# Kernel tuning notes

Hardware: AMD Instinct MI355X
Metric: run time of the kernel (lower is better)

## Reference

```python
import jax, jax.numpy as jnp
import numpy as np
from jax import lax

IMG_SIZE = 640
STRIDES = (8, 16, 32)
NA = 3          # anchors per level
NC = 80         # classes
CONF_THRESH = 0.001
NMS_THRESH = 0.6
ANCHORS = np.array([[10,13],[16,30],[33,23],[30,61],[62,45],[59,119],[116,90],[156,198],[373,326]], np.float32).reshape(3, 3, 2)

def _make_grids():
    gs, st, aw = [], [], []
    for i, s in enumerate(STRIDES):
        hs = ws = IMG_SIZE // s
        gy, gx = np.meshgrid(np.arange(hs), np.arange(ws), indexing='ij')
        gxy = np.stack([gx, gy], -1).astype(np.float32).reshape(1, hs*ws, 1, 2)
        gs.append(gxy)
        st.append(np.full((1, hs*ws, NA, 2), s, np.float32))
        aw.append(np.tile(ANCHORS[i][None], (hs*ws, 1, 1)))
    return (np.concatenate(gs, 1), np.concatenate(st, 1), np.concatenate(aw, 0)[None])

GRID_CELL, STRIDE_T, ANCH_WH = _make_grids()  # [1,HW,1,2], [1,HW,3,2], [1,HW,3,2]

def _nms_classaware(boxes, score, valid):
    # Greedy NMS, class-aware via coordinate offset already applied to boxes.
    # Faithful to the numpy baseline: w,h = max(1e-28, .), areas without +1.
    x1, y1, x2, y2 = boxes[:, 0], boxes[:, 1], boxes[:, 2], boxes[:, 3]
    areas = (x2 - x1) * (y2 - y1)
    order = jnp.argsort(-score)
    N = boxes.shape[0]
    def body(i, state):
        supp, keep = state
        idx = order[i]
        active = jnp.logical_and(jnp.logical_not(supp[idx]), valid[idx])
        keep = keep.at[idx].set(active)
        xx1 = jnp.maximum(x1[idx], x1)
        yy1 = jnp.maximum(y1[idx], y1)
        xx2 = jnp.minimum(x2[idx], x2)
        yy2 = jnp.minimum(y2[idx], y2)
        w = jnp.maximum(1e-28, xx2 - xx1)
        h = jnp.maximum(1e-28, yy2 - yy1)
        inter = w * h
        iou = inter / (areas[idx] + areas - inter)
        newsupp = jnp.logical_and(iou > NMS_THRESH, active)
        newsupp = newsupp.at[idx].set(False)
        return jnp.logical_or(supp, newsupp), keep
    supp0 = jnp.zeros((N,), bool)
    keep0 = jnp.zeros((N,), bool)
    _, keep = lax.fori_loop(0, N, body, (supp0, keep0))
    return keep

def _decode_and_nms(pred_s, pred_m, pred_l):
    objs, clss, regs = [], [], []
    for pred in (pred_s, pred_m, pred_l):
        B, C, H, W = pred.shape
        p = pred.transpose(0, 2, 3, 1).reshape(B, H*W, C)
        objs.append(p[..., :NA].reshape(B, H*W*NA, 1))
        clss.append(p[..., NA:NA*(1+NC)].reshape(B, H*W*NA, NC))
        regs.append(p[..., NA*(1+NC):].reshape(B, H*W, NA, 4))
    obj_pred = jnp.concatenate(objs, axis=1)   # [B, N, 1]
    cls_pred = jnp.concatenate(clss, axis=1)   # [B, N, NC]
    reg_pred = jnp.concatenate(regs, axis=1)   # [B, HW, 3, 4]
    grid = jnp.asarray(GRID_CELL)
    stride = jnp.asarray(STRIDE_T)
    anch = jnp.asarray(ANCH_WH)
    B = reg_pred.shape[0]
    c_xy = (jax.nn.sigmoid(reg_pred[..., :2]) + grid) * stride
    b_wh = jnp.exp(reg_pred[..., 2:]) * anch
    xywh = jnp.concatenate([c_xy, b_wh], -1).reshape(B, -1, 4)
    x1y1 = xywh[..., :2] - xywh[..., 2:] / 2
    x2y2 = xywh[..., :2] + xywh[..., 2:] / 2
    boxes = jnp.clip(jnp.concatenate([x1y1, x2y2], -1) / IMG_SIZE, 0.0, 1.0)[0]  # [N,4]
    obj_s = jax.nn.sigmoid(obj_pred)[0]                     # [N,1]
    scores_all = jax.nn.softmax(cls_pred[0], axis=1) * obj_s  # [N,NC]
    cls_ind = jnp.argmax(scores_all, axis=1)                # [N]
    score = jnp.max(scores_all, axis=1)                     # [N]
    valid = score >= CONF_THRESH
    # class-aware NMS: offset normalized boxes by 2*class so classes never overlap
    boxes_off = boxes + cls_ind[:, None].astype(boxes.dtype) * 2.0
    keep = _nms_classaware(lax.stop_gradient(boxes_off), lax.stop_gradient(score), valid)
    out = jnp.concatenate([
        boxes,                                    # 4 cols
        score[:, None],                           # 1 col
        cls_ind[:, None].astype(boxes.dtype),     # 1 col (non-diff)
        keep[:, None].astype(boxes.dtype),        # 1 col (non-diff)
    ], axis=1)                                    # [N, 7]
    return out

def setup_inputs() -> dict:
    key = jax.random.key(0)
    k1, k2, k3 = jax.random.split(key, 3)
    return {
        'pred_s': jax.random.normal(k1, (1, 255, 80, 80), jnp.float32),
        'pred_m': jax.random.normal(k2, (1, 255, 40, 40), jnp.float32),
        'pred_l': jax.random.normal(k3, (1, 255, 20, 20), jnp.float32),
    }

def reference(pred_s, pred_m, pred_l):
    return _decode_and_nms(pred_s, pred_m, pred_l)
```

## Files before the change

kernel.cpp:

```cpp
#include <hip/hip_runtime.h>
#include <cstdint>

#define NPRED 25200
#define NPOS  8400
#define NCLS  80
#define CAP   512
#define CSTRIDE 16
#define MW    8
#define NCHUNK 132

__device__ __forceinline__ float sigmoidf_(float x) { return 1.0f / (1.0f + expf(-x)); }

__global__ __launch_bounds__(64) void decode_kernel(
    const float* __restrict__ ps, const float* __restrict__ pm, const float* __restrict__ pl,
    float* __restrict__ out, int* __restrict__ counts,
    float4* __restrict__ g_boxin, uint64_t* __restrict__ g_key)
{
    int chunk = blockIdx.x;
    int a     = blockIdx.y;
    int t     = threadIdx.x;

    const float* p; int HW, W, base, si; float stride; int w0;
    if (chunk < 100)      { p = ps; HW = 6400; W = 80; stride = 8.f;  base = 0;    si = 0; w0 = chunk * 64; }
    else if (chunk < 125) { p = pm; HW = 1600; W = 40; stride = 16.f; base = 6400; si = 1; w0 = (chunk - 100) * 64; }
    else                  { p = pl; HW = 400;  W = 20; stride = 32.f; base = 8000; si = 2; w0 = (chunk - 125) * 64; }

    int local = w0 + t;
    bool valid = local < HW;
    int lclamp = valid ? local : (HW - 1);

    __shared__ float lds[NCLS * 64];

    const float* cbase = p + (size_t)(3 + a * NCLS) * HW;
    int lane_c = t >> 4;
    int j      = (t & 15) << 2;
    int off    = w0 + j; if (off > HW - 4) off = HW - 4;

    float4 vreg[20];
#pragma unroll
    for (int r0 = 0; r0 < 20; r0++)
        vreg[r0] = *(const float4*)(cbase + (size_t)(r0 * 4 + lane_c) * HW + off);
    float objl = p[(size_t)a * HW + lclamp];
    const float* rb = p + (size_t)(3 + 3 * NCLS + a * 4) * HW + lclamp;
    float tx = rb[0], ty = rb[(size_t)HW], tw = rb[(size_t)2 * HW], th = rb[(size_t)3 * HW];
#pragma unroll
    for (int r0 = 0; r0 < 20; r0++)
        *(float4*)&lds[(r0 * 4 + lane_c) * 64 + j] = vreg[r0];
    __syncthreads();

    float m = -INFINITY;
#pragma unroll 16
    for (int c = 0; c < NCLS; c++) m = fmaxf(m, lds[c * 64 + t]);
    float s = 0.f;
#pragma unroll 16
    for (int c = 0; c < NCLS; c++) {
        float e = expf(lds[c * 64 + t] - m);
        lds[c * 64 + t] = e;
        s += e;
    }
    float obj = sigmoidf_(objl);
    float best = -1.f; int bi = 0;
#pragma unroll 16
    for (int c = 0; c < NCLS; c++) {
        float sc = lds[c * 64 + t] / s * obj;
        if (sc > best) { best = sc; bi = c; }
    }

    if (!valid) return;

    const float AW[9] = {10.f,16.f,33.f, 30.f,62.f,59.f, 116.f,156.f,373.f};
    const float AH[9] = {13.f,30.f,23.f, 61.f,45.f,119.f, 90.f,198.f,326.f};
    float aw = AW[si*3 + a], ah = AH[si*3 + a];

    int y = local / W;
    int x = local - y * W;
    float cx = (sigmoidf_(tx) + (float)x) * stride;
    float cy = (sigmoidf_(ty) + (float)y) * stride;
    float bw = expf(tw) * aw;
    float bh = expf(th) * ah;
    float x1 = fminf(fmaxf((cx - bw / 2.f) / 640.f, 0.f), 1.f);
    float y1 = fminf(fmaxf((cy - bh / 2.f) / 640.f, 0.f), 1.f);
    float x2 = fminf(fmaxf((cx + bw / 2.f) / 640.f, 0.f), 1.f);
    float y2 = fminf(fmaxf((cy + bh / 2.f) / 640.f, 0.f), 1.f);

    int g = (base + local) * 3 + a;
    float clsf = (float)bi;
    float* o = out + (size_t)g * 7;
    o[0] = x1; o[1] = y1; o[2] = x2; o[3] = y2;
    o[4] = best; o[5] = clsf; o[6] = 0.f;

    if (best >= 0.001f) {
        int slot = atomicAdd(&counts[bi * CSTRIDE], 1);
        if (slot < CAP) {
            float off2 = clsf * 2.0f;
            g_boxin[bi * CAP + slot] = make_float4(x1 + off2, y1 + off2,
                                                   x2 + off2, y2 + off2);
            unsigned u = __float_as_uint(best);
            u = (u & 0x80000000u) ? ~u : (u | 0x80000000u);
            g_key[bi * CAP + slot] = ((uint64_t)(~u) << 15) | (uint64_t)g;
        }
    }
}

__global__ __launch_bounds__(1024) void nms_fused_kernel(
    const int* __restrict__ counts, const uint64_t* __restrict__ g_key,
    const float4* __restrict__ g_boxin, float* __restrict__ out)
{
    int c = blockIdx.x;
    int n = counts[c * CSTRIDE]; if (n > CAP) n = CAP;
    if (n == 0) return;
    int tid = threadIdx.x;
    int nw = (n + 63) >> 6;

    __shared__ uint64_t key_s[CAP];
    __shared__ float4   boxu_s[CAP];
    __shared__ float4   sbox_s[CAP + 64];
    __shared__ int      sg_s[CAP];
    __shared__ uint64_t mask_s[MW * CAP];

    for (int i = tid; i < n; i += 1024) {
        key_s[i]  = g_key[c * CAP + i];
        boxu_s[i] = g_boxin[c * CAP + i];
    }
    for (int i = n + tid; i < n + 64; i += 1024)
        sbox_s[i] = make_float4(3e30f, 3e30f, 3e30f, 3e30f);
    __syncthreads();

    for (int i0 = 0; i0 < n; i0 += 256) {
        int item = i0 + (tid >> 2);
        int sub  = tid & 3;
        bool act = item < n;
        int r = 0;
        uint64_t k = 0;
        if (act) {
            k = key_s[item];
            int nq = (n + 3) >> 2;
            int lo = sub * nq; if (lo > n) lo = n;
            int hi = lo + nq;  if (hi > n) hi = n;
            int jj = lo;
            for (; jj + 8 <= hi; jj += 8) {
                int t0 = key_s[jj]   < k, t1 = key_s[jj+1] < k;
                int t2 = key_s[jj+2] < k, t3 = key_s[jj+3] < k;
                int t4 = key_s[jj+4] < k, t5 = key_s[jj+5] < k;
                int t6 = key_s[jj+6] < k, t7 = key_s[jj+7] < k;
                r += t0 + t1 + t2 + t3 + t4 + t5 + t6 + t7;
            }
            for (; jj < hi; jj++) r += (key_s[jj] < k);
        }
        r += __shfl_xor(r, 1);
        r += __shfl_xor(r, 2);
        if (act && sub == 0) {
            sbox_s[r] = boxu_s[item];
            sg_s[r]   = (int)(k & 0x7FFF);
        }
    }
    __syncthreads();

    {
        int wid   = tid >> 6;
        int lane2 = tid & 63;
        int T = nw * (nw + 1) / 2;
        for (int t = wid; t < T; t += 16) {
            int w = 0, acc = 0;
            while (t >= acc + w + 1) { acc += w + 1; w++; }
            int ib = t - acc;
            int i  = (ib << 6) + lane2;
            float4 b4 = sbox_s[i];
            float Ai = (b4.z - b4.x) * (b4.w - b4.y);
            int j0 = w << 6;
            uint64_t bits = 0;
#pragma unroll 8
            for (int jq = 0; jq < 64; jq++) {
                float4 bj = sbox_s[j0 + jq];
                float xx1 = fmaxf(b4.x, bj.x);
                float yy1 = fmaxf(b4.y, bj.y);
                float xx2 = fminf(b4.z, bj.z);
                float yy2 = fminf(b4.w, bj.w);
                float ww = fmaxf(1e-28f, xx2 - xx1);
                float hh = fmaxf(1e-28f, yy2 - yy1);
                float inter = ww * hh;
                float Aj = (bj.z - bj.x) * (bj.w - bj.y);
                float iou = inter / ((Ai + Aj) - inter);
                if ((j0 + jq) > i && iou > 0.6f) bits |= 1ull << jq;
            }
            if (i < n) mask_s[w * CAP + i] = bits;
        }
    }
    __syncthreads();

    if (tid >= 64) return;
    int lane = tid;
    uint64_t removed = 0;
    for (int w = 0; w < nw; w++) {
        uint64_t rw = __shfl(removed, w);
        int row = (w << 6) + lane;
        uint64_t diag = (row < n) ? mask_s[w * CAP + row] : 0ull;
        int rem = n - (w << 6);
        uint64_t valid = (rem >= 64) ? ~0ull : ((1ull << rem) - 1ull);
        uint64_t nulls = __ballot(diag == 0ull);
        uint64_t cand = ~rw & valid;
        uint64_t kw = 0;
        uint64_t it = cand & ~nulls;
        while (it) {
            int b = __ffsll((unsigned long long)it) - 1;
            kw |= 1ull << b;
            uint64_t db = __shfl(diag, b);
            it &= ~db; cand &= ~db;
            it &= ~(1ull << b);
        }
        kw |= cand & nulls;

        int g  = lane >> 3;
        int wp = lane & 7;
        uint64_t acc = 0;
        if (wp >= w && wp < nw) {
            uint64_t mybits = kw & (0xFFull << (g * 8));
            while (mybits) {
                int b = __ffsll((unsigned long long)mybits) - 1;
                mybits &= mybits - 1;
                acc |= mask_s[wp * CAP + ((w << 6) + b)];
            }
        }
        acc |= __shfl_xor(acc, 8);
        acc |= __shfl_xor(acc, 16);
        acc |= __shfl_xor(acc, 32);
        if (lane < MW) removed |= acc;

        if (row < n && ((kw >> lane) & 1))
            out[(size_t)sg_s[row] * 7 + 6] = 1.0f;
    }
}

extern "C" void kernel_launch(void* const* d_in, const int* in_sizes, int n_in,
                              void* d_out, int out_size, void* d_ws, size_t ws_size,
                              hipStream_t stream) {
    const float* ps = (const float*)d_in[0];
    const float* pm = (const float*)d_in[1];
    const float* pl = (const float*)d_in[2];
    float* out = (float*)d_out;

    char* ws = (char*)d_ws;
    int*      counts  = (int*)ws;
    float4*   g_boxin = (float4*)(ws + 8192);
    uint64_t* g_key   = (uint64_t*)(ws + 663552);

    hipMemsetAsync(counts, 0, 8192, stream);
    decode_kernel<<<dim3(NCHUNK, 3), 64, 0, stream>>>(ps, pm, pl, out, counts, g_boxin, g_key);
    nms_fused_kernel<<<NCLS, 1024, 0, stream>>>(counts, g_key, g_boxin, out);
}
```

Baseline: 111.9 us.

## Replace global atomic class bucketing with per-class scan in NMS kernel

Decode now writes every prediction's key, with the class packed into the high bits, plus its box into dense arrays indexed by prediction id. This removes the global atomic counters and the memset launch. Each NMS block then scans all 25200 keys, compacts its own class into shared memory with an LDS atomic, and gathers boxes by index. The trade is one fewer launch and no global atomic contention, at the cost of every block reading the full key array (about 200KB per block, 80 blocks).

```diff
diff --git a/kernel.cpp b/kernel.cpp
--- a/kernel.cpp
+++ b/kernel.cpp
@@ -5,7 +5,6 @@
 #define NPOS  8400
 #define NCLS  80
 #define CAP   512
-#define CSTRIDE 16
 #define MW    8
 #define NCHUNK 132
 
@@ -13,7 +12,7 @@
 
 __global__ __launch_bounds__(64) void decode_kernel(
     const float* __restrict__ ps, const float* __restrict__ pm, const float* __restrict__ pl,
-    float* __restrict__ out, int* __restrict__ counts,
+    float* __restrict__ out,
     float4* __restrict__ g_boxin, uint64_t* __restrict__ g_key)
 {
     int chunk = blockIdx.x;
@@ -90,38 +89,47 @@
     o[4] = best; o[5] = clsf; o[6] = 0.f;
 
     if (best >= 0.001f) {
-        int slot = atomicAdd(&counts[bi * CSTRIDE], 1);
-        if (slot < CAP) {
-            float off2 = clsf * 2.0f;
-            g_boxin[bi * CAP + slot] = make_float4(x1 + off2, y1 + off2,
-                                                   x2 + off2, y2 + off2);
-            unsigned u = __float_as_uint(best);
-            u = (u & 0x80000000u) ? ~u : (u | 0x80000000u);
-            g_key[bi * CAP + slot] = ((uint64_t)(~u) << 15) | (uint64_t)g;
-        }
+        float off2 = clsf * 2.0f;
+        g_boxin[g] = make_float4(x1 + off2, y1 + off2, x2 + off2, y2 + off2);
+        unsigned u = __float_as_uint(best);
+        u = (u & 0x80000000u) ? ~u : (u | 0x80000000u);
+        g_key[g] = ((uint64_t)bi << 47) | ((uint64_t)(~u) << 15) | (uint64_t)g;
+    } else {
+        g_key[g] = (uint64_t)127 << 47;
     }
 }
 
 __global__ __launch_bounds__(1024) void nms_fused_kernel(
-    const int* __restrict__ counts, const uint64_t* __restrict__ g_key,
-    const float4* __restrict__ g_boxin, float* __restrict__ out)
+    const uint64_t* __restrict__ g_key, const float4* __restrict__ g_boxin,
+    float* __restrict__ out)
 {
     int c = blockIdx.x;
-    int n = counts[c * CSTRIDE]; if (n > CAP) n = CAP;
-    if (n == 0) return;
     int tid = threadIdx.x;
-    int nw = (n + 63) >> 6;
 
     __shared__ uint64_t key_s[CAP];
     __shared__ float4   boxu_s[CAP];
     __shared__ float4   sbox_s[CAP + 64];
     __shared__ int      sg_s[CAP];
     __shared__ uint64_t mask_s[MW * CAP];
-
-    for (int i = tid; i < n; i += 1024) {
-        key_s[i]  = g_key[c * CAP + i];
-        boxu_s[i] = g_boxin[c * CAP + i];
-    }
+    __shared__ int      ln_s;
+
+    if (tid == 0) ln_s = 0;
+    __syncthreads();
+
+    for (int idx = tid; idx < NPRED; idx += 1024) {
+        uint64_t k = g_key[idx];
+        if ((int)(k >> 47) == c) {
+            int slot = atomicAdd(&ln_s, 1);
+            if (slot < CAP) key_s[slot] = k;
+        }
+    }
+    __syncthreads();
+    int n = ln_s; if (n > CAP) n = CAP;
+    if (n == 0) return;
+    int nw = (n + 63) >> 6;
+
+    for (int i = tid; i < n; i += 1024)
+        boxu_s[i] = g_boxin[key_s[i] & 0x7FFF];
     for (int i = n + tid; i < n + 64; i += 1024)
         sbox_s[i] = make_float4(3e30f, 3e30f, 3e30f, 3e30f);
     __syncthreads();
@@ -240,11 +248,9 @@
     float* out = (float*)d_out;
 
     char* ws = (char*)d_ws;
-    int*      counts  = (int*)ws;
-    float4*   g_boxin = (float4*)(ws + 8192);
-    uint64_t* g_key   = (uint64_t*)(ws + 663552);
-
-    hipMemsetAsync(counts, 0, 8192, stream);
-    decode_kernel<<<dim3(NCHUNK, 3), 64, 0, stream>>>(ps, pm, pl, out, counts, g_boxin, g_key);
-    nms_fused_kernel<<<NCLS, 1024, 0, stream>>>(counts, g_key, g_boxin, out);
+    float4*   g_boxin = (float4*)ws;
+    uint64_t* g_key   = (uint64_t*)(ws + 409600);
+
+    decode_kernel<<<dim3(NCHUNK, 3), 64, 0, stream>>>(ps, pm, pl, out, g_boxin, g_key);
+    nms_fused_kernel<<<NCLS, 1024, 0, stream>>>(g_key, g_boxin, out);
 }
```

After: 112.8 us. No clear change (+0.9%).
